# Performance work log

Hardware: AMD Instinct MI355X
Metric: run time of the kernel (lower is better)

Reference implementation:

```python
import jax, jax.numpy as jnp
import numpy as np

INTERVAL = 4
UPSCALE = 4
K = 3              # sample_size
SAMPLERS = 3
Q = 2 ** INTERVAL                 # 16
L = 2 ** (8 - INTERVAL) + 1       # 17
PAD = K - 1
B, H, W = 4, 512, 512

_STRIDES = np.array([L ** 3, L ** 2, L, 1], dtype=np.int32)


def ste_round(x):
    # straight-through round (round_func in the torch code)
    return x + jax.lax.stop_gradient(jnp.round(x) - x)


def fix_weight(w):
    return jnp.clip(ste_round(w * 127.0), -127.0, 127.0)


def sample(img, sw, sb):
    # unfold(K, K-1) + conv-per-patch + fold is exactly a VALID conv.
    # img: (B,1,h+PAD,w+PAD); sw: (4,1,K,K) -> a,b,c,d each (B,1,h,w)
    out = jax.lax.conv_general_dilated(img, sw, (1, 1), 'VALID',
        dimension_numbers=('NCHW', 'OIHW', 'NCHW')) + sb[None, :, None, None]
    return out[:, 0:1], out[:, 1:2], out[:, 2:3], out[:, 3:4]


def interp(lut, res_w, sw, sb, scale, img_in, prev_img):
    # InterpTorchBatch: 4D simplex interpolation into the quantized LUT.
    # Sorted-simplex form is equivalent to the 24-case masked torch code
    # (ties yield zero-weight terms, so tie ordering is irrelevant).
    w = fix_weight(lut)                                       # (L^4, scale*scale)
    a, b, c, d = sample(img_in, sw, sb)
    if prev_img is not None:
        rw = jnp.clip(res_w, 0.0, 1.0)
        pa, pb, pc, pd = sample(prev_img, sw, sb)
        a = rw[0, 0] * pa + (1.0 - rw[0, 0]) * a
        b = rw[0, 1] * pb + (1.0 - rw[0, 1]) * b
        c = rw[1, 0] * pc + (1.0 - rw[1, 0]) * c
        d = rw[1, 1] * pd + (1.0 - rw[1, 1]) * d
    vals = jnp.concatenate([a, b, c, d], axis=1).transpose(0, 2, 3, 1)   # (B,h,w,4)
    lo = jnp.floor_divide(vals, float(Q)).astype(jnp.int32)
    f = jnp.mod(vals, float(Q))
    order = jnp.argsort(-f, axis=-1)                          # fractional parts, descending
    fs = jnp.take_along_axis(f, order, axis=-1)
    strides = jnp.asarray(_STRIDES)
    base = jnp.sum(lo * strides, axis=-1)                     # flat index of p0000
    inc = jnp.cumsum(strides[order], axis=-1)
    verts = jnp.concatenate([base[..., None], base[..., None] + inc], axis=-1)  # (B,h,w,5)
    ws = jnp.concatenate([float(Q) - fs[..., :1], fs[..., :-1] - fs[..., 1:], fs[..., -1:]], axis=-1)
    p = w[verts]                                              # gather: (B,h,w,5,scale*scale)
    out = jnp.einsum('bhwv,bhwvk->bhwk', ws, p) / float(Q)
    bb, hh, ww, _ = out.shape
    out = out.reshape(bb, hh, ww, scale, scale).transpose(0, 1, 3, 2, 4)
    return out.reshape(bb, 1, hh * scale, ww * scale)


def _pad_rot(x, r):
    return jnp.pad(jnp.rot90(x, r, axes=(2, 3)),
                   ((0, 0), (0, 0), (0, PAD), (0, PAD)), mode='edge')


def rotate_input(lut, scale, sw, sb, x, res_w, prev_x):
    pred = jnp.zeros((), jnp.float32)
    for r in range(4):
        pr = None if prev_x is None else _pad_rot(prev_x, r)
        pred = pred + jnp.rot90(
            interp(lut, res_w, sw, sb, scale, _pad_rot(x, r), pr),
            (4 - r) % 4, axes=(2, 3))
        pred = ste_round(pred)
    return pred


def autolut_forward(x, lut0, lut1, samp0, samp1, sbias0, sbias1, resw1):
    x = x * 255.0
    # stage 0: scale 1, no residual, bias 127
    pred = 0.0
    for s in range(SAMPLERS):
        pred = pred + rotate_input(lut0[s], 1, samp0[s], sbias0[s], x, None, None)
    prev_x = x
    x = ste_round(jnp.clip(pred / (SAMPLERS * 4.0) + 127.0, 0.0, 255.0))
    # stage 1 (last): upscale, residual blend with previous stage input
    pred = 0.0
    for s in range(SAMPLERS):
        pred = pred + rotate_input(lut1[s], UPSCALE, samp1[s], sbias1[s], x, resw1[s], prev_x)
    x = ste_round(jnp.clip(pred / float(SAMPLERS), 0.0, 255.0))
    return x / 255.0   # phase == 'train'


def setup_inputs() -> dict:
    key = jax.random.key(0)
    ks = jax.random.split(key, 6)
    x = jax.random.uniform(ks[0], (B, 1, H, W), dtype=jnp.float32)
    lut0 = jax.random.uniform(ks[1], (SAMPLERS, L ** 4, 1), jnp.float32, -1.0, 1.0)
    lut1 = jax.random.uniform(ks[2], (SAMPLERS, L ** 4, UPSCALE * UPSCALE), jnp.float32, -1.0, 1.0)

    def mk_sampler(k):
        w = jax.random.normal(k, (SAMPLERS, 4, 1, K, K), dtype=jnp.float32)
        # convex combination of patch pixels -> sampled values stay in [0,255]
        return jax.nn.softmax(w.reshape(SAMPLERS, 4, -1), axis=-1).reshape(SAMPLERS, 4, 1, K, K)

    samp0 = mk_sampler(ks[3])
    samp1 = mk_sampler(ks[4])
    sbias0 = jnp.zeros((SAMPLERS, 4), jnp.float32)
    sbias1 = jnp.zeros((SAMPLERS, 4), jnp.float32)
    resw1 = jax.random.uniform(ks[5], (SAMPLERS, 2, 2), dtype=jnp.float32)
    return {"x": x, "lut0": lut0, "lut1": lut1, "samp0": samp0, "samp1": samp1,
            "sbias0": sbias0, "sbias1": sbias1, "resw1": resw1}


def reference(x, lut0, lut1, samp0, samp1, sbias0, sbias1, resw1):
    return autolut_forward(x, lut0, lut1, samp0, samp1, sbias0, sbias1, resw1)
```

## Files before the change

kernel.cpp:

```cpp
#include <hip/hip_runtime.h>
#include <math.h>

static constexpr int B_ = 4;
static constexpr int N_ = 512;
static constexpr int N4_ = 2048;
static constexpr int NPIX = B_ * N_ * N_;
static constexpr int LUT_ROWS = 83521;
static constexpr int SPAD = 83584;
static constexpr int ST0 = 4913, ST1 = 289, ST2 = 17, ST3 = 1;

__device__ __forceinline__ float fixw(float v) {
    v = rintf(v * 127.0f);
    return fminf(fmaxf(v, -127.0f), 127.0f);
}

__global__ void fix_lut0_kernel(const float* __restrict__ in, char* __restrict__ out) {
    int t = blockIdx.x * blockDim.x + threadIdx.x;
    int s = blockIdx.y;
    if (t < LUT_ROWS) out[(size_t)s * SPAD + t] = (char)(int)fixw(in[(size_t)s * LUT_ROWS + t]);
}

__global__ void fix_lut1_kernel(const float4* __restrict__ in, uchar4* __restrict__ out, int n4) {
    int t = blockIdx.x * blockDim.x + threadIdx.x;
    if (t < n4) {
        float4 v = in[t];
        uchar4 o;
        o.x = (unsigned char)((int)fixw(v.x) + 127);
        o.y = (unsigned char)((int)fixw(v.y) + 127);
        o.z = (unsigned char)((int)fixw(v.z) + 127);
        o.w = (unsigned char)((int)fixw(v.w) + 127);
        out[t] = o;
    }
}

struct Simplex {
    int v[5];
    float w[5];
};

__device__ __forceinline__ Simplex simplex4(float a, float b, float c, float d) {
    float fl0 = floorf(a * 0.0625f), fl1 = floorf(b * 0.0625f),
          fl2 = floorf(c * 0.0625f), fl3 = floorf(d * 0.0625f);
    float f[4] = { a - 16.0f * fl0, b - 16.0f * fl1, c - 16.0f * fl2, d - 16.0f * fl3 };
    int l0 = min(max((int)fl0, 0), 15);
    int l1 = min(max((int)fl1, 0), 15);
    int l2 = min(max((int)fl2, 0), 15);
    int l3 = min(max((int)fl3, 0), 15);
    int st[4] = { ST0, ST1, ST2, ST3 };
#define CSW(A, Bq) { if (f[A] < f[Bq]) { float tf = f[A]; f[A] = f[Bq]; f[Bq] = tf; \
                                         int ts = st[A]; st[A] = st[Bq]; st[Bq] = ts; } }
    CSW(0, 1) CSW(1, 2) CSW(2, 3) CSW(0, 1) CSW(1, 2) CSW(0, 1)
#undef CSW
    Simplex s;
    s.v[0] = l0 * ST0 + l1 * ST1 + l2 * ST2 + l3;
    s.v[1] = s.v[0] + st[0];
    s.v[2] = s.v[1] + st[1];
    s.v[3] = s.v[2] + st[2];
    s.v[4] = s.v[3] + st[3];
    s.w[0] = (16.0f - f[0]) * 0.0625f;
    s.w[1] = (f[0] - f[1]) * 0.0625f;
    s.w[2] = (f[1] - f[2]) * 0.0625f;
    s.w[3] = (f[2] - f[3]) * 0.0625f;
    s.w[4] = f[3] * 0.0625f;
    return s;
}

__device__ __forceinline__ bool tap_for_r(int r, int a, int c, int& di, int& dj) {
    if (r == 0) { di = a - 2; dj = c - 2; return (a >= 2) && (c >= 2); }
    if (r == 1) { di = 2 - c; dj = a - 2; return (a >= 2) && (c <= 2); }
    if (r == 2) { di = 2 - a; dj = 2 - c; return (a <= 2) && (c <= 2); }
    di = c - 2; dj = 2 - a; return (a <= 2) && (c >= 2);
}

__device__ __forceinline__ void acc4u(unsigned int q, float wv, float* oc) {
    oc[0] = fmaf(wv, (float)(q & 0xffu), oc[0]);
    oc[1] = fmaf(wv, (float)((q >> 8) & 0xffu), oc[1]);
    oc[2] = fmaf(wv, (float)((q >> 16) & 0xffu), oc[2]);
    oc[3] = fmaf(wv, (float)(q >> 24), oc[3]);
}

__global__ __launch_bounds__(1024, 4) void stage0_kernel(
    const float* __restrict__ x,
    const char* __restrict__ lut0q,
    const float* __restrict__ samp0,
    const float* __restrict__ sbias0,
    float* __restrict__ x1)
{
    __shared__ char luts[SPAD];

    int b    = blockIdx.x >> 8;
    int tile = blockIdx.x & 255;
    int i = ((tile >> 4) << 5) + (threadIdx.x >> 5);
    int j = ((tile & 15) << 5) + (threadIdx.x & 31);
    const float* xb = x + (size_t)b * N_ * N_;

    float pred = 0.0f;
    for (int s = 0; s < 3; ++s) {
        __syncthreads();
        {
            const int4* src = (const int4*)(lut0q + (size_t)s * SPAD);
            int4* dst = (int4*)luts;
            for (int u = threadIdx.x; u < SPAD / 16; u += 1024) dst[u] = src[u];
        }
        __syncthreads();

        const float* w  = samp0 + s * 36;
        const float* sb = sbias0 + s * 4;

        float vals[4][4];
        #pragma unroll
        for (int r = 0; r < 4; ++r)
            #pragma unroll
            for (int ch = 0; ch < 4; ++ch) vals[r][ch] = 0.0f;
        #pragma unroll
        for (int a = 0; a < 5; ++a) {
            int ri = min(max(i - 2 + a, 0), N_ - 1);
            #pragma unroll
            for (int c = 0; c < 5; ++c) {
                int ci = min(max(j - 2 + c, 0), N_ - 1);
                float px = xb[ri * N_ + ci] * 255.0f;
                #pragma unroll
                for (int r = 0; r < 4; ++r) {
                    int di, dj;
                    if (tap_for_r(r, a, c, di, dj)) {
                        #pragma unroll
                        for (int ch = 0; ch < 4; ++ch)
                            vals[r][ch] += w[ch * 9 + di * 3 + dj] * px;
                    }
                }
            }
        }

        float acc = 0.0f;
        #pragma unroll
        for (int r = 0; r < 4; ++r) {
            Simplex sx = simplex4(vals[r][0] + sb[0], vals[r][1] + sb[1],
                                  vals[r][2] + sb[2], vals[r][3] + sb[3]);
            float p0 = (float)luts[sx.v[0]];
            float p1 = (float)luts[sx.v[1]];
            float p2 = (float)luts[sx.v[2]];
            float p3 = (float)luts[sx.v[3]];
            float p4 = (float)luts[sx.v[4]];
            float o = sx.w[0] * p0 + sx.w[1] * p1 + sx.w[2] * p2
                    + sx.w[3] * p3 + sx.w[4] * p4;
            acc = rintf(acc + o);
        }
        pred += acc;
    }
    x1[(size_t)b * N_ * N_ + i * N_ + j] =
        rintf(fminf(fmaxf(pred / 12.0f + 127.0f, 0.0f), 255.0f));
}

__global__ __launch_bounds__(256) void stage1_kernel(
    const float* __restrict__ x,
    const float* __restrict__ x1,
    const unsigned char* __restrict__ lut1q,
    const float* __restrict__ samp1,
    const float* __restrict__ sbias1,
    const float* __restrict__ resw1,
    float* __restrict__ out)
{
    int b    = blockIdx.x >> 10;
    int tile = blockIdx.x & 1023;
    int i = ((tile >> 5) << 4) + (threadIdx.x >> 4);
    int j = ((tile & 31) << 4) + (threadIdx.x & 15);
    const float* xb  = x  + (size_t)b * N_ * N_;
    const float* x1b = x1 + (size_t)b * N_ * N_;

    float tot[16];
    #pragma unroll
    for (int k = 0; k < 16; ++k) tot[k] = 0.0f;

    for (int s = 0; s < 3; ++s) {
        const float* w  = samp1 + s * 36;
        const float* sb = sbias1 + s * 4;
        const unsigned char* lut = lut1q + (size_t)s * LUT_ROWS * 16;
        float rw[4];
        #pragma unroll
        for (int ch = 0; ch < 4; ++ch)
            rw[ch] = fminf(fmaxf(resw1[s * 4 + ch], 0.0f), 1.0f);

        float vals[4][4];
        {
            float vc[4][4], vp[4][4];
            #pragma unroll
            for (int r = 0; r < 4; ++r)
                #pragma unroll
                for (int ch = 0; ch < 4; ++ch) { vc[r][ch] = 0.0f; vp[r][ch] = 0.0f; }
            #pragma unroll
            for (int a = 0; a < 5; ++a) {
                int ri = min(max(i - 2 + a, 0), N_ - 1);
                #pragma unroll
                for (int c = 0; c < 5; ++c) {
                    int ci = min(max(j - 2 + c, 0), N_ - 1);
                    float pc = x1b[ri * N_ + ci];
                    float pp = xb[ri * N_ + ci] * 255.0f;
                    #pragma unroll
                    for (int r = 0; r < 4; ++r) {
                        int di, dj;
                        if (tap_for_r(r, a, c, di, dj)) {
                            #pragma unroll
                            for (int ch = 0; ch < 4; ++ch) {
                                float wt = w[ch * 9 + di * 3 + dj];
                                vc[r][ch] += wt * pc;
                                vp[r][ch] += wt * pp;
                            }
                        }
                    }
                }
            }
            #pragma unroll
            for (int r = 0; r < 4; ++r)
                #pragma unroll
                for (int ch = 0; ch < 4; ++ch)
                    vals[r][ch] = rw[ch] * (vp[r][ch] + sb[ch])
                                + (1.0f - rw[ch]) * (vc[r][ch] + sb[ch]);
        }

        float acc[16];
        #pragma unroll
        for (int k = 0; k < 16; ++k) acc[k] = 0.0f;

        #pragma unroll
        for (int r = 0; r < 4; ++r) {
            Simplex sx = simplex4(vals[r][0], vals[r][1], vals[r][2], vals[r][3]);
            float oc[16];
            #pragma unroll
            for (int k = 0; k < 16; ++k) oc[k] = 0.0f;
            #pragma unroll
            for (int v = 0; v < 5; ++v) {
                const uint4 q = *(const uint4*)(lut + (size_t)sx.v[v] * 16);
                float wv = sx.w[v];
                acc4u(q.x, wv, oc);
                acc4u(q.y, wv, oc + 4);
                acc4u(q.z, wv, oc + 8);
                acc4u(q.w, wv, oc + 12);
            }
            float S = sx.w[0] + sx.w[1] + sx.w[2] + sx.w[3] + sx.w[4];
            float bias = 127.0f * S;
            #pragma unroll
            for (int k = 0; k < 16; ++k) oc[k] -= bias;
            #pragma unroll
            for (int u = 0; u < 4; ++u)
                #pragma unroll
                for (int v2 = 0; v2 < 4; ++v2) {
                    int k = 4 * u + v2;
                    int c = (r == 0) ? (4 * u + v2)
                          : (r == 1) ? (4 * (3 - v2) + u)
                          : (r == 2) ? (4 * (3 - u) + (3 - v2))
                                     : (4 * v2 + (3 - u));
                    acc[k] = rintf(acc[k] + oc[c]);
                }
        }
        #pragma unroll
        for (int k = 0; k < 16; ++k) tot[k] += acc[k];
    }

    float* ob = out + (size_t)b * N4_ * N4_ + (size_t)(i * 4) * N4_ + (j * 4);
    #pragma unroll
    for (int u = 0; u < 4; ++u) {
        float4 val;
        val.x = rintf(fminf(fmaxf(tot[4 * u + 0] / 3.0f, 0.0f), 255.0f)) * (1.0f / 255.0f);
        val.y = rintf(fminf(fmaxf(tot[4 * u + 1] / 3.0f, 0.0f), 255.0f)) * (1.0f / 255.0f);
        val.z = rintf(fminf(fmaxf(tot[4 * u + 2] / 3.0f, 0.0f), 255.0f)) * (1.0f / 255.0f);
        val.w = rintf(fminf(fmaxf(tot[4 * u + 3] / 3.0f, 0.0f), 255.0f)) * (1.0f / 255.0f);
        *(float4*)(ob + (size_t)u * N4_) = val;
    }
}

extern "C" void kernel_launch(void* const* d_in, const int* in_sizes, int n_in,
                              void* d_out, int out_size, void* d_ws, size_t ws_size,
                              hipStream_t stream) {
    const float* x      = (const float*)d_in[0];
    const float* lut0   = (const float*)d_in[1];
    const float* lut1   = (const float*)d_in[2];
    const float* samp0  = (const float*)d_in[3];
    const float* samp1  = (const float*)d_in[4];
    const float* sbias0 = (const float*)d_in[5];
    const float* sbias1 = (const float*)d_in[6];
    const float* resw1  = (const float*)d_in[7];
    float* out = (float*)d_out;
    char* ws   = (char*)d_ws;

    const int N_L1 = 3 * LUT_ROWS * 16;
    size_t off_x1 = 0;
    size_t off_l0 = (size_t)NPIX * sizeof(float);
    size_t off_l1 = (off_l0 + (size_t)3 * SPAD + 15) & ~(size_t)15;

    float* x1 = (float*)(ws + off_x1);
    char* l0q = ws + off_l0;
    unsigned char* l1q = (unsigned char*)(ws + off_l1);

    const int threads = 256;

    dim3 g0((LUT_ROWS + threads - 1) / threads, 3);
    fix_lut0_kernel<<<g0, threads, 0, stream>>>(lut0, l0q);
    fix_lut1_kernel<<<(N_L1 / 4 + threads - 1) / threads, threads, 0, stream>>>(
        (const float4*)lut1, (uchar4*)l1q, N_L1 / 4);
    stage0_kernel<<<NPIX / 1024, 1024, 0, stream>>>(x, l0q, samp0, sbias0, x1);
    stage1_kernel<<<NPIX / threads, threads, 0, stream>>>(x, x1, l1q, samp1, sbias1, resw1, out);
}
```

Baseline: 296.7 us.

## Fuse stage0 and stage1 into one kernel with shared-memory halo tiles

Merges the two pixel stages into a single kernel. Each 16x16 output tile loads a 24x24 halo of x into shared memory and computes a 20x20 stage-0 tile (x1) into LDS, so stage 1 reads x and x1 from shared memory and the global round trip for x1 goes away. The cost is recomputing about 56% more stage-0 pixels for the halo. The lut0 lookups now go to global/L1 memory instead of the LDS-resident table, and only 400 of 768 thread-slots do stage-0 work in an unbalanced second pass.

```diff
diff --git a/kernel.cpp b/kernel.cpp
--- a/kernel.cpp
+++ b/kernel.cpp
@@ -79,93 +79,88 @@
     oc[3] = fmaf(wv, (float)(q >> 24), oc[3]);
 }
 
-__global__ __launch_bounds__(1024, 4) void stage0_kernel(
+__global__ __launch_bounds__(256) void fused_kernel(
     const float* __restrict__ x,
     const char* __restrict__ lut0q,
-    const float* __restrict__ samp0,
-    const float* __restrict__ sbias0,
-    float* __restrict__ x1)
-{
-    __shared__ char luts[SPAD];
-
-    int b    = blockIdx.x >> 8;
-    int tile = blockIdx.x & 255;
-    int i = ((tile >> 4) << 5) + (threadIdx.x >> 5);
-    int j = ((tile & 15) << 5) + (threadIdx.x & 31);
-    const float* xb = x + (size_t)b * N_ * N_;
-
-    float pred = 0.0f;
-    for (int s = 0; s < 3; ++s) {
-        __syncthreads();
-        {
-            const int4* src = (const int4*)(lut0q + (size_t)s * SPAD);
-            int4* dst = (int4*)luts;
-            for (int u = threadIdx.x; u < SPAD / 16; u += 1024) dst[u] = src[u];
-        }
-        __syncthreads();
-
-        const float* w  = samp0 + s * 36;
-        const float* sb = sbias0 + s * 4;
-
-        float vals[4][4];
-        #pragma unroll
-        for (int r = 0; r < 4; ++r)
-            #pragma unroll
-            for (int ch = 0; ch < 4; ++ch) vals[r][ch] = 0.0f;
-        #pragma unroll
-        for (int a = 0; a < 5; ++a) {
-            int ri = min(max(i - 2 + a, 0), N_ - 1);
-            #pragma unroll
-            for (int c = 0; c < 5; ++c) {
-                int ci = min(max(j - 2 + c, 0), N_ - 1);
-                float px = xb[ri * N_ + ci] * 255.0f;
-                #pragma unroll
-                for (int r = 0; r < 4; ++r) {
-                    int di, dj;
-                    if (tap_for_r(r, a, c, di, dj)) {
-                        #pragma unroll
-                        for (int ch = 0; ch < 4; ++ch)
-                            vals[r][ch] += w[ch * 9 + di * 3 + dj] * px;
-                    }
-                }
-            }
-        }
-
-        float acc = 0.0f;
-        #pragma unroll
-        for (int r = 0; r < 4; ++r) {
-            Simplex sx = simplex4(vals[r][0] + sb[0], vals[r][1] + sb[1],
-                                  vals[r][2] + sb[2], vals[r][3] + sb[3]);
-            float p0 = (float)luts[sx.v[0]];
-            float p1 = (float)luts[sx.v[1]];
-            float p2 = (float)luts[sx.v[2]];
-            float p3 = (float)luts[sx.v[3]];
-            float p4 = (float)luts[sx.v[4]];
-            float o = sx.w[0] * p0 + sx.w[1] * p1 + sx.w[2] * p2
-                    + sx.w[3] * p3 + sx.w[4] * p4;
-            acc = rintf(acc + o);
-        }
-        pred += acc;
-    }
-    x1[(size_t)b * N_ * N_ + i * N_ + j] =
-        rintf(fminf(fmaxf(pred / 12.0f + 127.0f, 0.0f), 255.0f));
-}
-
-__global__ __launch_bounds__(256) void stage1_kernel(
-    const float* __restrict__ x,
-    const float* __restrict__ x1,
     const unsigned char* __restrict__ lut1q,
-    const float* __restrict__ samp1,
-    const float* __restrict__ sbias1,
+    const float* __restrict__ samp0,  const float* __restrict__ sbias0,
+    const float* __restrict__ samp1,  const float* __restrict__ sbias1,
     const float* __restrict__ resw1,
     float* __restrict__ out)
 {
+    __shared__ float xh[24][25];
+    __shared__ float x1h[20][21];
+
     int b    = blockIdx.x >> 10;
     int tile = blockIdx.x & 1023;
-    int i = ((tile >> 5) << 4) + (threadIdx.x >> 4);
-    int j = ((tile & 31) << 4) + (threadIdx.x & 15);
-    const float* xb  = x  + (size_t)b * N_ * N_;
-    const float* x1b = x1 + (size_t)b * N_ * N_;
+    int ti = ((tile >> 5) << 4);
+    int tj = ((tile & 31) << 4);
+    const float* xb = x + (size_t)b * N_ * N_;
+
+    for (int p = threadIdx.x; p < 576; p += 256) {
+        int qi = p / 24, qj = p - qi * 24;
+        int gi = min(max(ti - 4 + qi, 0), N_ - 1);
+        int gj = min(max(tj - 4 + qj, 0), N_ - 1);
+        xh[qi][qj] = xb[gi * N_ + gj];
+    }
+    __syncthreads();
+
+    for (int p = threadIdx.x; p < 400; p += 256) {
+        int pi = p / 20, pj = p - pi * 20;
+        int hi = min(max(ti - 2 + pi, 0), N_ - 1);
+        int hj = min(max(tj - 2 + pj, 0), N_ - 1);
+
+        float pred = 0.0f;
+        for (int s = 0; s < 3; ++s) {
+            const float* w  = samp0 + s * 36;
+            const float* sb = sbias0 + s * 4;
+            const char* lut = lut0q + (size_t)s * SPAD;
+
+            float vals[4][4];
+            #pragma unroll
+            for (int r = 0; r < 4; ++r)
+                #pragma unroll
+                for (int ch = 0; ch < 4; ++ch) vals[r][ch] = 0.0f;
+            #pragma unroll
+            for (int a = 0; a < 5; ++a) {
+                int ra = min(max(hi - 2 + a, 0), N_ - 1) - (ti - 4);
+                #pragma unroll
+                for (int c = 0; c < 5; ++c) {
+                    int ca = min(max(hj - 2 + c, 0), N_ - 1) - (tj - 4);
+                    float px = xh[ra][ca] * 255.0f;
+                    #pragma unroll
+                    for (int r = 0; r < 4; ++r) {
+                        int di, dj;
+                        if (tap_for_r(r, a, c, di, dj)) {
+                            #pragma unroll
+                            for (int ch = 0; ch < 4; ++ch)
+                                vals[r][ch] += w[ch * 9 + di * 3 + dj] * px;
+                        }
+                    }
+                }
+            }
+            float acc = 0.0f;
+            #pragma unroll
+            for (int r = 0; r < 4; ++r) {
+                Simplex sx = simplex4(vals[r][0] + sb[0], vals[r][1] + sb[1],
+                                      vals[r][2] + sb[2], vals[r][3] + sb[3]);
+                float p0 = (float)lut[sx.v[0]];
+                float p1 = (float)lut[sx.v[1]];
+                float p2 = (float)lut[sx.v[2]];
+                float p3 = (float)lut[sx.v[3]];
+                float p4 = (float)lut[sx.v[4]];
+                float o = sx.w[0] * p0 + sx.w[1] * p1 + sx.w[2] * p2
+                        + sx.w[3] * p3 + sx.w[4] * p4;
+                acc = rintf(acc + o);
+            }
+            pred += acc;
+        }
+        x1h[pi][pj] = rintf(fminf(fmaxf(pred / 12.0f + 127.0f, 0.0f), 255.0f));
+    }
+    __syncthreads();
+
+    int u = threadIdx.x >> 4, v = threadIdx.x & 15;
+    int i = ti + u, j = tj + v;
 
     float tot[16];
     #pragma unroll
@@ -190,11 +185,13 @@
             #pragma unroll
             for (int a = 0; a < 5; ++a) {
                 int ri = min(max(i - 2 + a, 0), N_ - 1);
+                int r1 = ri - (ti - 2);
+                int r2 = ri - (ti - 4);
                 #pragma unroll
                 for (int c = 0; c < 5; ++c) {
                     int ci = min(max(j - 2 + c, 0), N_ - 1);
-                    float pc = x1b[ri * N_ + ci];
-                    float pp = xb[ri * N_ + ci] * 255.0f;
+                    float pc = x1h[r1][ci - (tj - 2)];
+                    float pp = xh[r2][ci - (tj - 4)] * 255.0f;
                     #pragma unroll
                     for (int r = 0; r < 4; ++r) {
                         int di, dj;
@@ -228,9 +225,9 @@
             #pragma unroll
             for (int k = 0; k < 16; ++k) oc[k] = 0.0f;
             #pragma unroll
-            for (int v = 0; v < 5; ++v) {
-                const uint4 q = *(const uint4*)(lut + (size_t)sx.v[v] * 16);
-                float wv = sx.w[v];
+            for (int vv = 0; vv < 5; ++vv) {
+                const uint4 q = *(const uint4*)(lut + (size_t)sx.v[vv] * 16);
+                float wv = sx.w[vv];
                 acc4u(q.x, wv, oc);
                 acc4u(q.y, wv, oc + 4);
                 acc4u(q.z, wv, oc + 8);
@@ -241,14 +238,14 @@
             #pragma unroll
             for (int k = 0; k < 16; ++k) oc[k] -= bias;
             #pragma unroll
-            for (int u = 0; u < 4; ++u)
+            for (int u2 = 0; u2 < 4; ++u2)
                 #pragma unroll
                 for (int v2 = 0; v2 < 4; ++v2) {
-                    int k = 4 * u + v2;
-                    int c = (r == 0) ? (4 * u + v2)
-                          : (r == 1) ? (4 * (3 - v2) + u)
-                          : (r == 2) ? (4 * (3 - u) + (3 - v2))
-                                     : (4 * v2 + (3 - u));
+                    int k = 4 * u2 + v2;
+                    int c = (r == 0) ? (4 * u2 + v2)
+                          : (r == 1) ? (4 * (3 - v2) + u2)
+                          : (r == 2) ? (4 * (3 - u2) + (3 - v2))
+                                     : (4 * v2 + (3 - u2));
                     acc[k] = rintf(acc[k] + oc[c]);
                 }
         }
@@ -258,13 +255,13 @@
 
     float* ob = out + (size_t)b * N4_ * N4_ + (size_t)(i * 4) * N4_ + (j * 4);
     #pragma unroll
-    for (int u = 0; u < 4; ++u) {
+    for (int u2 = 0; u2 < 4; ++u2) {
         float4 val;
-        val.x = rintf(fminf(fmaxf(tot[4 * u + 0] / 3.0f, 0.0f), 255.0f)) * (1.0f / 255.0f);
-        val.y = rintf(fminf(fmaxf(tot[4 * u + 1] / 3.0f, 0.0f), 255.0f)) * (1.0f / 255.0f);
-        val.z = rintf(fminf(fmaxf(tot[4 * u + 2] / 3.0f, 0.0f), 255.0f)) * (1.0f / 255.0f);
-        val.w = rintf(fminf(fmaxf(tot[4 * u + 3] / 3.0f, 0.0f), 255.0f)) * (1.0f / 255.0f);
-        *(float4*)(ob + (size_t)u * N4_) = val;
+        val.x = rintf(fminf(fmaxf(tot[4 * u2 + 0] / 3.0f, 0.0f), 255.0f)) * (1.0f / 255.0f);
+        val.y = rintf(fminf(fmaxf(tot[4 * u2 + 1] / 3.0f, 0.0f), 255.0f)) * (1.0f / 255.0f);
+        val.z = rintf(fminf(fmaxf(tot[4 * u2 + 2] / 3.0f, 0.0f), 255.0f)) * (1.0f / 255.0f);
+        val.w = rintf(fminf(fmaxf(tot[4 * u2 + 3] / 3.0f, 0.0f), 255.0f)) * (1.0f / 255.0f);
+        *(float4*)(ob + (size_t)u2 * N4_) = val;
     }
 }
 
@@ -283,11 +280,9 @@
     char* ws   = (char*)d_ws;
 
     const int N_L1 = 3 * LUT_ROWS * 16;
-    size_t off_x1 = 0;
-    size_t off_l0 = (size_t)NPIX * sizeof(float);
-    size_t off_l1 = (off_l0 + (size_t)3 * SPAD + 15) & ~(size_t)15;
-
-    float* x1 = (float*)(ws + off_x1);
+    size_t off_l0 = 0;
+    size_t off_l1 = ((size_t)3 * SPAD + 15) & ~(size_t)15;
+
     char* l0q = ws + off_l0;
     unsigned char* l1q = (unsigned char*)(ws + off_l1);
 
@@ -297,6 +292,6 @@
     fix_lut0_kernel<<<g0, threads, 0, stream>>>(lut0, l0q);
     fix_lut1_kernel<<<(N_L1 / 4 + threads - 1) / threads, threads, 0, stream>>>(
         (const float4*)lut1, (uchar4*)l1q, N_L1 / 4);
-    stage0_kernel<<<NPIX / 1024, 1024, 0, stream>>>(x, l0q, samp0, sbias0, x1);
-    stage1_kernel<<<NPIX / threads, threads, 0, stream>>>(x, x1, l1q, samp1, sbias1, resw1, out);
-}
+    fused_kernel<<<NPIX / threads, threads, 0, stream>>>(
+        x, l0q, l1q, samp0, sbias0, samp1, sbias1, resw1, out);
+}
```

Measured after the change: 351.3 us. +18.4%, slower.
